# Kernel optimization log

Hardware: AMD Instinct MI355X
Metric: run time of the kernel (lower is better)

Reference implementation:

```python
import jax, jax.numpy as jnp
import numpy as np

B, L, D, H = 16, 4096, 512, 512
TEMP, THRESH, PRIOR = 1.0, 0.5, 0.25


def setup_inputs() -> dict:
    key = jax.random.key(0)
    k1, k2, k3, k4, k5 = jax.random.split(key, 5)
    hidden = jax.random.normal(k1, (B, L, D), jnp.float32)
    # variable-length sequences: lengths in [L/2, L]
    lengths = jax.random.randint(k2, (B,), L // 2, L + 1)
    attention_mask = (jnp.arange(L)[None, :] < lengths[:, None]).astype(jnp.float32)
    # uniform noise for RelaxedBernoulli rsample (logistic reparameterization)
    u = jax.random.uniform(k3, (B, L), jnp.float32, 1e-6, 1.0 - 1e-6)
    w1 = jax.random.normal(k4, (D, H), jnp.float32) * (1.0 / np.sqrt(D))
    b1 = jnp.zeros((H,), jnp.float32)
    w2 = jax.random.normal(k5, (H, 1), jnp.float32) * (1.0 / np.sqrt(H))
    b2 = jnp.full((1,), 3.0, jnp.float32)  # init_for_12: bias filled with +3
    return dict(hidden=hidden, attention_mask=attention_mask, u=u,
                w1=w1, b1=b1, w2=w2, b2=b2)


def _binomial_loss(k, n, p):
    # -log Binomial(n, p).pmf(k) / n
    log_coef = (jax.lax.lgamma(n + 1.0) - jax.lax.lgamma(k + 1.0)
                - jax.lax.lgamma(n - k + 1.0))
    return -(log_coef + k * jnp.log(p) + (n - k) * jnp.log1p(-p)) / n


def _forward(hidden, attention_mask, u, w1, b1, w2, b2):
    # boundary MLP -> logits (B, L)
    logits = (jax.nn.relu(hidden @ w1 + b1) @ w2 + b2)[..., 0]
    # RelaxedBernoulli(temp, probs=sigmoid(logits)).rsample():
    # sigmoid((logits + logistic_noise) / temp)
    logistic = jnp.log(u) - jnp.log1p(-u)
    soft = jax.nn.sigmoid((logits + logistic) / TEMP) * attention_mask
    hard = (soft > THRESH).astype(hidden.dtype) * attention_mask
    # force a boundary on the last real token of each sequence
    pad = attention_mask == 0
    first_pad = pad & (jnp.cumsum(pad.astype(jnp.int32), axis=1) == 1)
    last_real = jnp.roll(first_pad, -1, axis=1).at[:, -1].set(False).astype(hidden.dtype)
    hard = jnp.maximum(hard, last_real)
    soft = jnp.maximum(soft, last_real)
    # straight-through estimator
    hard_b = hard - jax.lax.stop_gradient(soft) + soft
    masked_hidden = hidden * attention_mask[..., None]
    # segment id of token t = #boundaries strictly before t (boundary closes its segment)
    hard_sg = jax.lax.stop_gradient(hard)
    seg = (jnp.cumsum(hard_sg, axis=1) - hard_sg).astype(jnp.int32)  # (B, L)

    def pool_one(x, sid):
        # x: (L, D), sid: (L,) -> mean pool per segment, padded to L segments
        s = jax.ops.segment_sum(x, sid, num_segments=L)
        c = jax.ops.segment_sum(jnp.ones((L,), x.dtype), sid, num_segments=L)
        return s / jnp.maximum(c, 1.0)[:, None]

    pooled = jax.vmap(pool_one)(masked_hidden, seg)  # (B, L, D), first nb[b] rows valid
    nb = hard_sg.sum(axis=1)  # per-example boundary count
    valid = jnp.arange(L)[None, :] < nb[:, None]
    pooled = pooled * valid[..., None]
    shortened_attention_mask = valid.astype(attention_mask.dtype)  # padded to L
    k = hard_b.sum()
    n = attention_mask.sum()
    loss = _binomial_loss(k, n, PRIOR)
    return pooled, loss, k, n, shortened_attention_mask


def reference(hidden, attention_mask, u, w1, b1, w2, b2):
    return _forward(hidden, attention_mask, u, w1, b1, w2, b2)
```

## Files before the change

kernel.cpp:

```cpp
#include <hip/hip_runtime.h>
#include <hip/hip_bf16.h>
#include <stdint.h>

#define BB 16
#define LL 4096
#define DD 512
#define HH 512
#define MM (BB * LL)
#define NTILES_H 8

typedef _Float16 f16x8 __attribute__((ext_vector_type(8)));
typedef float f32x4 __attribute__((ext_vector_type(4)));


__global__ __launch_bounds__(256) void conv_a_kernel(
    const float* __restrict__ A, _Float16* __restrict__ Ah, _Float16* __restrict__ Al)
{
    const int t    = blockIdx.x * 256 + threadIdx.x;
    const int tile = t >> 9;
    const int u    = t & 511;
    const int ml   = u >> 2;
    const int q    = u & 3;
    const int mt   = tile >> 4;
    const int kt   = tile & 15;
    const int g    = q ^ (ml & 3);

    const float* src = A + ((size_t)(mt * 128 + ml)) * DD + kt * 32;
    const float4 x = *reinterpret_cast<const float4*>(src + 4 * g);
    const float4 y = *reinterpret_cast<const float4*>(src + 16 + 4 * g);
    const float v[8] = {x.x, x.y, x.z, x.w, y.x, y.y, y.z, y.w};

    f16x8 h, l;
#pragma unroll
    for (int e = 0; e < 8; ++e) {
        const _Float16 hh = (_Float16)v[e];
        const float r = v[e] - (float)hh;
        h[e] = hh;
        l[e] = (_Float16)(r * 4096.0f);
    }
    *reinterpret_cast<f16x8*>(Ah + (size_t)tile * 4096 + u * 8) = h;
    *reinterpret_cast<f16x8*>(Al + (size_t)tile * 4096 + u * 8) = l;
}

__global__ __launch_bounds__(256) void conv_b_kernel(
    const float* __restrict__ W1, _Float16* __restrict__ Bh, _Float16* __restrict__ Bl)
{
    const int t    = blockIdx.x * 256 + threadIdx.x;
    const int tile = t >> 9;
    const int u    = t & 511;
    const int nl   = u >> 2;
    const int q    = u & 3;
    const int ht   = tile >> 4;
    const int kt   = tile & 15;
    const int g    = q ^ (nl & 3);

    const int n = ht * 128 + nl;
    const int kbase = kt * 32;
    f16x8 h, l;
#pragma unroll
    for (int e = 0; e < 8; ++e) {
        const int k = kbase + ((e < 4) ? (4 * g + e) : (16 + 4 * g + (e - 4)));
        const float v = W1[(size_t)k * HH + n] * 64.0f;
        const _Float16 hh = (_Float16)v;
        const float r = v - (float)hh;
        h[e] = hh;
        l[e] = (_Float16)(r * 4096.0f);
    }
    *reinterpret_cast<f16x8*>(Bh + (size_t)tile * 4096 + u * 8) = h;
    *reinterpret_cast<f16x8*>(Bl + (size_t)tile * 4096 + u * 8) = l;
}

__device__ __forceinline__ void gload16(const void* g, void* l)
{
    __builtin_amdgcn_global_load_lds(
        (const __attribute__((address_space(1))) unsigned int*)g,
        (__attribute__((address_space(3))) unsigned int*)l, 16, 0, 0);
}

__global__ __launch_bounds__(256, 2) void gemm_mfma_kernel(
    const _Float16* __restrict__ Ah, const _Float16* __restrict__ Al,
    const _Float16* __restrict__ Bh, const _Float16* __restrict__ Bl,
    const float* __restrict__ B1,    const float* __restrict__ W2,
    float* __restrict__ part)
{
    __shared__ __align__(16) char lds[2][4][8192];

    const int d  = blockIdx.x;
    const int x  = d & 7;
    const int ht = (d >> 3) & 3;
    const int mt = x * 64 + (d >> 5);

    const int tid  = threadIdx.x;
    const int lane = tid & 63;
    const int w    = tid >> 6;
    const int wr   = w >> 1;
    const int wc   = w & 1;
    const int c    = lane & 15;
    const int g    = lane >> 4;

    int aoff[4], boff[4];
#pragma unroll
    for (int f = 0; f < 4; ++f) {
        const int m_local = wr * 64 + f * 16 + c;
        aoff[f] = m_local * 64 + ((g ^ (c & 3)) << 4);
        const int n_local = wc * 64 + f * 16 + c;
        boff[f] = n_local * 64 + ((g ^ (c & 3)) << 4);
    }

    f32x4 accM[4][4] = {};
    f32x4 accL[4][4] = {};

    auto stage = [&](int kt, int b) {
        const _Float16* s0 = Ah + ((size_t)(mt * 16 + kt)) * 4096;
        const _Float16* s1 = Al + ((size_t)(mt * 16 + kt)) * 4096;
        const _Float16* s2 = Bh + ((size_t)(ht * 16 + kt)) * 4096;
        const _Float16* s3 = Bl + ((size_t)(ht * 16 + kt)) * 4096;
        char* l = &lds[b][0][0];
#pragma unroll
        for (int i = 0; i < 2; ++i) {
            const int e = (tid + i * 256) * 8;
            const int o = (tid + i * 256) * 16;
            gload16(s0 + e, l + 0 * 8192 + o);
            gload16(s1 + e, l + 1 * 8192 + o);
            gload16(s2 + e, l + 2 * 8192 + o);
            gload16(s3 + e, l + 3 * 8192 + o);
        }
    };

    stage(0, 0);
    int buf = 0;
    for (int kt = 0; kt < 16; ++kt) {
        __syncthreads();
        if (kt + 1 < 16) stage(kt + 1, buf ^ 1);
        const char* base = &lds[buf][0][0];
        f16x8 ah[4], al[4];
#pragma unroll
        for (int mf = 0; mf < 4; ++mf) {
            ah[mf] = *reinterpret_cast<const f16x8*>(base + 0 * 8192 + aoff[mf]);
            al[mf] = *reinterpret_cast<const f16x8*>(base + 1 * 8192 + aoff[mf]);
        }
#pragma unroll
        for (int nf = 0; nf < 4; ++nf) {
            const f16x8 bh = *reinterpret_cast<const f16x8*>(base + 2 * 8192 + boff[nf]);
            const f16x8 bl = *reinterpret_cast<const f16x8*>(base + 3 * 8192 + boff[nf]);
#pragma unroll
            for (int mf = 0; mf < 4; ++mf) {
                accM[mf][nf] = __builtin_amdgcn_mfma_f32_16x16x32_f16(ah[mf], bh, accM[mf][nf], 0, 0, 0);
                accL[mf][nf] = __builtin_amdgcn_mfma_f32_16x16x32_f16(ah[mf], bl, accL[mf][nf], 0, 0, 0);
                accL[mf][nf] = __builtin_amdgcn_mfma_f32_16x16x32_f16(al[mf], bh, accL[mf][nf], 0, 0, 0);
            }
        }
        buf ^= 1;
    }

    float w2v[4], b1v[4];
#pragma unroll
    for (int nf = 0; nf < 4; ++nf) {
        const int n = ht * 128 + wc * 64 + nf * 16 + c;
        w2v[nf] = W2[n];
        b1v[nf] = B1[n];
    }
    float red[4][4];
#pragma unroll
    for (int mf = 0; mf < 4; ++mf)
#pragma unroll
        for (int r = 0; r < 4; ++r) {
            float s = 0.0f;
#pragma unroll
            for (int nf = 0; nf < 4; ++nf) {
                float y = (accM[mf][nf][r] + accL[mf][nf][r] * (1.0f / 4096.0f)) * (1.0f / 64.0f) + b1v[nf];
                y = (y > 0.0f) ? y : 0.0f;
                s = fmaf(y, w2v[nf], s);
            }
            red[mf][r] = s;
        }
#pragma unroll
    for (int step = 1; step < 16; step <<= 1)
#pragma unroll
        for (int mf = 0; mf < 4; ++mf)
#pragma unroll
            for (int r = 0; r < 4; ++r)
                red[mf][r] += __shfl_xor(red[mf][r], step);
    if (c == 0) {
        const int p = ht * 2 + wc;
#pragma unroll
        for (int mf = 0; mf < 4; ++mf)
#pragma unroll
            for (int r = 0; r < 4; ++r) {
                const int m = mt * 128 + wr * 64 + mf * 16 + g * 4 + r;
                part[(size_t)p * MM + m] = red[mf][r];
            }
    }
}

#define BM 64
#define BN 64
#define BK 32

__global__ __launch_bounds__(256) void mlp_gemm_kernel(
    const float* __restrict__ A, const float* __restrict__ W1,
    const float* __restrict__ B1, const float* __restrict__ W2,
    float* __restrict__ part)
{
    __shared__ __align__(16) float As[BK][BM];
    __shared__ __align__(16) float Bs[BK][BN];
    __shared__ float red[64][17];

    const int ht = blockIdx.x;
    const int mt = blockIdx.y;
    const int t  = threadIdx.x;
    const int tx = t & 15;
    const int ty = t >> 4;
    const int row0 = mt * BM;
    const int n0   = ht * BN;

    float acc[4][4];
#pragma unroll
    for (int i = 0; i < 4; ++i)
#pragma unroll
        for (int j = 0; j < 4; ++j) acc[i][j] = 0.0f;

    for (int k0 = 0; k0 < DD; k0 += BK) {
#pragma unroll
        for (int i = 0; i < 2; ++i) {
            const int idx = t + i * 256;
            const int m   = idx >> 3;
            const int kq  = idx & 7;
            const float4 a = *reinterpret_cast<const float4*>(
                &A[(size_t)(row0 + m) * DD + k0 + kq * 4]);
            As[kq * 4 + 0][m] = a.x;
            As[kq * 4 + 1][m] = a.y;
            As[kq * 4 + 2][m] = a.z;
            As[kq * 4 + 3][m] = a.w;
        }
#pragma unroll
        for (int i = 0; i < 2; ++i) {
            const int idx = t + i * 256;
            const int kk  = idx >> 4;
            const int nq  = idx & 15;
            const float4 bv = *reinterpret_cast<const float4*>(
                &W1[(size_t)(k0 + kk) * HH + n0 + nq * 4]);
            *reinterpret_cast<float4*>(&Bs[kk][nq * 4]) = bv;
        }
        __syncthreads();
#pragma unroll
        for (int k = 0; k < BK; ++k) {
            const float4 av = *reinterpret_cast<const float4*>(&As[k][ty * 4]);
            const float4 bv = *reinterpret_cast<const float4*>(&Bs[k][tx * 4]);
            const float a[4]  = {av.x, av.y, av.z, av.w};
            const float bb[4] = {bv.x, bv.y, bv.z, bv.w};
#pragma unroll
            for (int i = 0; i < 4; ++i)
#pragma unroll
                for (int j = 0; j < 4; ++j)
                    acc[i][j] = fmaf(a[i], bb[j], acc[i][j]);
        }
        __syncthreads();
    }

    const float4 b1v = *reinterpret_cast<const float4*>(&B1[n0 + tx * 4]);
    const float4 w2v = *reinterpret_cast<const float4*>(&W2[n0 + tx * 4]);
    const float b1a[4] = {b1v.x, b1v.y, b1v.z, b1v.w};
    const float w2a[4] = {w2v.x, w2v.y, w2v.z, w2v.w};
#pragma unroll
    for (int i = 0; i < 4; ++i) {
        float p = 0.0f;
#pragma unroll
        for (int j = 0; j < 4; ++j) {
            float y = acc[i][j] + b1a[j];
            y = (y > 0.0f) ? y : 0.0f;
            p = fmaf(y, w2a[j], p);
        }
        red[ty * 4 + i][tx] = p;
    }
    __syncthreads();
    if (t < 64) {
        float s = 0.0f;
#pragma unroll
        for (int q = 0; q < 16; ++q) s += red[t][q];
        part[(size_t)(t & 0) * 0 + (size_t)blockIdx.x * MM + row0 + t] = s;
    }
}

__global__ __launch_bounds__(1024) void boundary_scan_kernel(
    const float* __restrict__ part, const float* __restrict__ mask,
    const float* __restrict__ u,    const float* __restrict__ b2,
    int* __restrict__ bpos, int* __restrict__ nb, int* __restrict__ lenb,
    float* __restrict__ smask_out)
{
    __shared__ int sdata[1024];
    __shared__ int s_len;
    const int b   = blockIdx.x;
    const int tid = threadIdx.x;
    const int base = b * LL;
    const float b2v = b2[0];

    float mv[4];
    int lm = 0;
#pragma unroll
    for (int j = 0; j < 4; ++j) {
        const int l = tid * 4 + j;
        mv[j] = mask[base + l];
        lm += (mv[j] != 0.0f) ? 1 : 0;
    }
    sdata[tid] = lm;
    __syncthreads();
    for (int off = 512; off > 0; off >>= 1) {
        if (tid < off) sdata[tid] += sdata[tid + off];
        __syncthreads();
    }
    if (tid == 0) s_len = sdata[0];
    __syncthreads();
    const int len = s_len;
    __syncthreads();

    int h[4];
    int cnt = 0;
#pragma unroll
    for (int j = 0; j < 4; ++j) {
        const int l = tid * 4 + j;
        float logit = b2v;
#pragma unroll
        for (int p = 0; p < NTILES_H; ++p) logit += part[(size_t)p * MM + base + l];
        const float uu = u[base + l];
        const float xx = logit + logf(uu) - log1pf(-uu);
        int hh = (xx > 0.0f && mv[j] != 0.0f) ? 1 : 0;
        if (len < LL && l == len - 1) hh = 1;
        h[j] = hh;
        cnt += hh;
    }

    sdata[tid] = cnt;
    __syncthreads();
    for (int off = 1; off < 1024; off <<= 1) {
        int v = (tid >= off) ? sdata[tid - off] : 0;
        __syncthreads();
        sdata[tid] += v;
        __syncthreads();
    }
    const int excl  = sdata[tid] - cnt;
    const int total = sdata[1023];

    int pos = excl;
#pragma unroll
    for (int j = 0; j < 4; ++j) {
        if (h[j]) {
            bpos[base + pos] = tid * 4 + j;
            ++pos;
        }
    }
    if (tid == 0) {
        nb[b]   = total;
        lenb[b] = len;
    }
#pragma unroll
    for (int j = 0; j < 4; ++j) {
        const int l = tid * 4 + j;
        smask_out[base + l] = (l < total) ? 1.0f : 0.0f;
    }
}

__global__ __launch_bounds__(128) void pool_kernel(
    const float* __restrict__ hidden, const int* __restrict__ bpos,
    const int* __restrict__ nb, float* __restrict__ out)
{
    const int blk = blockIdx.x;
    const int b   = blk >> 12;
    const int s   = blk & (LL - 1);
    const int tid = threadIdx.x;
    const int base = b * LL;

    float ax = 0.0f, ay = 0.0f, az = 0.0f, aw = 0.0f;
    const int n = nb[b];
    if (s < n) {
        const int start = (s == 0) ? 0 : (bpos[base + s - 1] + 1);
        const int end   = bpos[base + s];
        const float inv = 1.0f / (float)(end - start + 1);
        for (int tkn = start; tkn <= end; ++tkn) {
            const float4 v = *reinterpret_cast<const float4*>(
                &hidden[((size_t)(base + tkn)) * DD + tid * 4]);
            ax += v.x; ay += v.y; az += v.z; aw += v.w;
        }
        ax *= inv; ay *= inv; az *= inv; aw *= inv;
    }
    float4 r; r.x = ax; r.y = ay; r.z = az; r.w = aw;
    *reinterpret_cast<float4*>(&out[((size_t)(base + s)) * DD + tid * 4]) = r;
}

__global__ void finalize_kernel(
    const int* __restrict__ nb, const int* __restrict__ lenb,
    float* __restrict__ out)
{
    if (threadIdx.x == 0 && blockIdx.x == 0) {
        int k = 0, n = 0;
        for (int b = 0; b < BB; ++b) { k += nb[b]; n += lenb[b]; }
        const double dk = (double)k, dn = (double)n, p = 0.25;
        const double logc = lgamma(dn + 1.0) - lgamma(dk + 1.0) - lgamma(dn - dk + 1.0);
        const double loss = -(logc + dk * log(p) + (dn - dk) * log1p(-p)) / dn;
        out[0] = (float)loss;
        out[1] = (float)k;
        out[2] = (float)n;
    }
}

extern "C" void kernel_launch(void* const* d_in, const int* in_sizes, int n_in,
                              void* d_out, int out_size, void* d_ws, size_t ws_size,
                              hipStream_t stream) {
    const float* hidden = (const float*)d_in[0];
    const float* mask   = (const float*)d_in[1];
    const float* u      = (const float*)d_in[2];
    const float* w1     = (const float*)d_in[3];
    const float* b1     = (const float*)d_in[4];
    const float* w2     = (const float*)d_in[5];
    const float* b2     = (const float*)d_in[6];
    float* out = (float*)d_out;

    const size_t AH_BYTES = (size_t)8192 * 4096 * 2;
    const size_t BH_BYTES = (size_t)64 * 4096 * 2;
    const size_t PART_BYTES = (size_t)NTILES_H * MM * 4;
    const size_t BPOS_BYTES = (size_t)MM * 4;
    const size_t need = AH_BYTES * 2 + BH_BYTES * 2 + PART_BYTES + BPOS_BYTES + 128;

    const size_t P = (size_t)MM * DD;
    float* smask = out + P + 3;

    char* ws = (char*)d_ws;
    float* part; int* bpos; int* nbuf; int* lenb;

    if (ws_size >= need) {
        _Float16* Ah = (_Float16*)ws;
        _Float16* Al = (_Float16*)(ws + AH_BYTES);
        _Float16* Bh = (_Float16*)(ws + AH_BYTES * 2);
        _Float16* Bl = (_Float16*)(ws + AH_BYTES * 2 + BH_BYTES);
        part = (float*)(ws + AH_BYTES * 2 + BH_BYTES * 2);
        bpos = (int*)(ws + AH_BYTES * 2 + BH_BYTES * 2 + PART_BYTES);
        nbuf = (int*)(ws + AH_BYTES * 2 + BH_BYTES * 2 + PART_BYTES + BPOS_BYTES);
        lenb = nbuf + BB;

        conv_a_kernel<<<16384, 256, 0, stream>>>(hidden, Ah, Al);
        conv_b_kernel<<<128, 256, 0, stream>>>(w1, Bh, Bl);
        gemm_mfma_kernel<<<2048, 256, 0, stream>>>(Ah, Al, Bh, Bl, b1, w2, part);
    } else {
        part = (float*)ws;
        bpos = (int*)(ws + PART_BYTES);
        nbuf = (int*)(ws + PART_BYTES + BPOS_BYTES);
        lenb = nbuf + BB;
        mlp_gemm_kernel<<<dim3(NTILES_H, MM / BM), 256, 0, stream>>>(hidden, w1, b1, w2, part);
    }

    boundary_scan_kernel<<<BB, 1024, 0, stream>>>(part, mask, u, b2, bpos, nbuf, lenb, smask);
    pool_kernel<<<MM, 128, 0, stream>>>(hidden, bpos, nbuf, out);
    finalize_kernel<<<1, 64, 0, stream>>>(nbuf, lenb, out + P);
}
```

Before: 398.2 us.

## Parallelize boundary scan across chunks and strengthen LDS swizzle for MFMA tiles

The single-block-per-sequence boundary scan is replaced by three kernels. A binary-search length kernel finds each sequence length. A 256-block flags kernel computes hard boundaries with per-chunk ballot counts. A 256-block scan kernel compacts boundary positions using chunk prefix sums and wave ballots. This aims to remove the long, serial-ish 1024-thread Hillis-Steele scan that ran on only 16 blocks. Separately, the fp16 tile swizzle gains an extra XOR term in both the conversion kernels and the GEMM LDS addressing, to reduce LDS bank conflicts. The binary search relies on the mask being a contiguous prefix of ones.

```diff
diff --git a/kernel.cpp b/kernel.cpp
--- a/kernel.cpp
+++ b/kernel.cpp
@@ -23,7 +23,7 @@
     const int q    = u & 3;
     const int mt   = tile >> 4;
     const int kt   = tile & 15;
-    const int g    = q ^ (ml & 3);
+    const int g    = q ^ (ml & 3) ^ ((ml >> 2) & 3);
 
     const float* src = A + ((size_t)(mt * 128 + ml)) * DD + kt * 32;
     const float4 x = *reinterpret_cast<const float4*>(src + 4 * g);
@@ -52,7 +52,7 @@
     const int q    = u & 3;
     const int ht   = tile >> 4;
     const int kt   = tile & 15;
-    const int g    = q ^ (nl & 3);
+    const int g    = q ^ (nl & 3) ^ ((nl >> 2) & 3);
 
     const int n = ht * 128 + nl;
     const int kbase = kt * 32;
@@ -98,13 +98,14 @@
     const int c    = lane & 15;
     const int g    = lane >> 4;
 
+    const int q = g ^ (c & 3) ^ ((c >> 2) & 3);
     int aoff[4], boff[4];
 #pragma unroll
     for (int f = 0; f < 4; ++f) {
         const int m_local = wr * 64 + f * 16 + c;
-        aoff[f] = m_local * 64 + ((g ^ (c & 3)) << 4);
+        aoff[f] = m_local * 64 + (q << 4);
         const int n_local = wc * 64 + f * 16 + c;
-        boff[f] = n_local * 64 + ((g ^ (c & 3)) << 4);
+        boff[f] = n_local * 64 + (q << 4);
     }
 
     f32x4 accM[4][4] = {};
@@ -278,86 +279,94 @@
         float s = 0.0f;
 #pragma unroll
         for (int q = 0; q < 16; ++q) s += red[t][q];
-        part[(size_t)(t & 0) * 0 + (size_t)blockIdx.x * MM + row0 + t] = s;
-    }
-}
-
-__global__ __launch_bounds__(1024) void boundary_scan_kernel(
-    const float* __restrict__ part, const float* __restrict__ mask,
-    const float* __restrict__ u,    const float* __restrict__ b2,
-    int* __restrict__ bpos, int* __restrict__ nb, int* __restrict__ lenb,
-    float* __restrict__ smask_out)
-{
-    __shared__ int sdata[1024];
-    __shared__ int s_len;
-    const int b   = blockIdx.x;
-    const int tid = threadIdx.x;
-    const int base = b * LL;
-    const float b2v = b2[0];
-
-    float mv[4];
-    int lm = 0;
-#pragma unroll
-    for (int j = 0; j < 4; ++j) {
-        const int l = tid * 4 + j;
-        mv[j] = mask[base + l];
-        lm += (mv[j] != 0.0f) ? 1 : 0;
-    }
-    sdata[tid] = lm;
+        part[(size_t)ht * MM + row0 + t] = s;
+    }
+}
+
+
+__global__ void len_kernel(const float* __restrict__ mask, int* __restrict__ lenb)
+{
+    const int b = threadIdx.x;
+    if (b < BB) {
+        const float* row = mask + b * LL;
+        int lo = 0, hi = LL;
+        while (lo < hi) {
+            const int mid = (lo + hi) >> 1;
+            if (row[mid] == 0.0f) hi = mid; else lo = mid + 1;
+        }
+        lenb[b] = lo;
+    }
+}
+
+__global__ __launch_bounds__(256) void flags_kernel(
+    const float* __restrict__ part, const float* __restrict__ u,
+    const float* __restrict__ b2,   const int* __restrict__ lenb,
+    int* __restrict__ flags, int* __restrict__ chunkcnt)
+{
+    __shared__ int wsum[4];
+    const int m   = blockIdx.x * 256 + threadIdx.x;
+    const int b   = m >> 12;
+    const int l   = m & (LL - 1);
+    const int len = lenb[b];
+
+    float logit = b2[0];
+#pragma unroll
+    for (int p = 0; p < NTILES_H; ++p) logit += part[(size_t)p * MM + m];
+    const float uu = u[m];
+    const float xx = logit + logf(uu) - log1pf(-uu);
+
+    int hh = (xx > 0.0f && l < len) ? 1 : 0;
+    if (len < LL && l == len - 1) hh = 1;
+    flags[m] = hh;
+
+    const unsigned long long bal = __ballot(hh);
+    const int lane = threadIdx.x & 63;
+    const int wid  = threadIdx.x >> 6;
+    if (lane == 0) wsum[wid] = __popcll(bal);
     __syncthreads();
-    for (int off = 512; off > 0; off >>= 1) {
-        if (tid < off) sdata[tid] += sdata[tid + off];
-        __syncthreads();
-    }
-    if (tid == 0) s_len = sdata[0];
+    if (threadIdx.x == 0)
+        chunkcnt[blockIdx.x] = wsum[0] + wsum[1] + wsum[2] + wsum[3];
+}
+
+__global__ __launch_bounds__(256) void scan_kernel(
+    const int* __restrict__ flags, const int* __restrict__ chunkcnt,
+    int* __restrict__ bpos, int* __restrict__ nb, float* __restrict__ smask_out)
+{
+    __shared__ int s_chunk[16];
+    __shared__ int wsum[4];
+    const int bid   = blockIdx.x;
+    const int b     = bid >> 4;
+    const int chunk = bid & 15;
+    const int tid   = threadIdx.x;
+    const int m     = bid * 256 + tid;
+    const int l     = m & (LL - 1);
+
+    if (tid < 16) s_chunk[tid] = chunkcnt[b * 16 + tid];
+
+    const int hh = flags[m];
+    const unsigned long long bal = __ballot(hh);
+    const int lane = tid & 63;
+    const int wid  = tid >> 6;
+    if (lane == 0) wsum[wid] = __popcll(bal);
     __syncthreads();
-    const int len = s_len;
-    __syncthreads();
-
-    int h[4];
-    int cnt = 0;
-#pragma unroll
-    for (int j = 0; j < 4; ++j) {
-        const int l = tid * 4 + j;
-        float logit = b2v;
-#pragma unroll
-        for (int p = 0; p < NTILES_H; ++p) logit += part[(size_t)p * MM + base + l];
-        const float uu = u[base + l];
-        const float xx = logit + logf(uu) - log1pf(-uu);
-        int hh = (xx > 0.0f && mv[j] != 0.0f) ? 1 : 0;
-        if (len < LL && l == len - 1) hh = 1;
-        h[j] = hh;
-        cnt += hh;
-    }
-
-    sdata[tid] = cnt;
-    __syncthreads();
-    for (int off = 1; off < 1024; off <<= 1) {
-        int v = (tid >= off) ? sdata[tid - off] : 0;
-        __syncthreads();
-        sdata[tid] += v;
-        __syncthreads();
-    }
-    const int excl  = sdata[tid] - cnt;
-    const int total = sdata[1023];
-
-    int pos = excl;
-#pragma unroll
-    for (int j = 0; j < 4; ++j) {
-        if (h[j]) {
-            bpos[base + pos] = tid * 4 + j;
-            ++pos;
-        }
-    }
-    if (tid == 0) {
-        nb[b]   = total;
-        lenb[b] = len;
-    }
-#pragma unroll
-    for (int j = 0; j < 4; ++j) {
-        const int l = tid * 4 + j;
-        smask_out[base + l] = (l < total) ? 1.0f : 0.0f;
-    }
+
+    int pre = 0, tot = 0;
+#pragma unroll
+    for (int i = 0; i < 16; ++i) {
+        const int ci = s_chunk[i];
+        pre += (i < chunk) ? ci : 0;
+        tot += ci;
+    }
+    int woff = 0;
+#pragma unroll
+    for (int i = 0; i < 4; ++i) woff += (i < wid) ? wsum[i] : 0;
+
+    if (hh) {
+        const int excl = __popcll(bal & ((1ull << lane) - 1ull));
+        bpos[b * LL + pre + woff + excl] = l;
+    }
+    smask_out[m] = (l < tot) ? 1.0f : 0.0f;
+    if (chunk == 0 && tid == 0) nb[b] = tot;
 }
 
 __global__ __launch_bounds__(128) void pool_kernel(
@@ -415,40 +424,46 @@
     const float* b2     = (const float*)d_in[6];
     float* out = (float*)d_out;
 
-    const size_t AH_BYTES = (size_t)8192 * 4096 * 2;
-    const size_t BH_BYTES = (size_t)64 * 4096 * 2;
+    const size_t AH_BYTES   = (size_t)8192 * 4096 * 2;
+    const size_t BH_BYTES   = (size_t)64 * 4096 * 2;
     const size_t PART_BYTES = (size_t)NTILES_H * MM * 4;
     const size_t BPOS_BYTES = (size_t)MM * 4;
-    const size_t need = AH_BYTES * 2 + BH_BYTES * 2 + PART_BYTES + BPOS_BYTES + 128;
+    const size_t FLAG_BYTES = (size_t)MM * 4;
+    const size_t need = AH_BYTES * 2 + BH_BYTES * 2 + PART_BYTES + BPOS_BYTES + FLAG_BYTES + 4096;
 
     const size_t P = (size_t)MM * DD;
     float* smask = out + P + 3;
 
     char* ws = (char*)d_ws;
-    float* part; int* bpos; int* nbuf; int* lenb;
-
-    if (ws_size >= need) {
+    float* part; int* bpos; int* flags; int* chunkcnt; int* nbuf; int* lenb;
+    bool fast = (ws_size >= need);
+
+    char* tail;
+    if (fast) tail = ws + AH_BYTES * 2 + BH_BYTES * 2;
+    else      tail = ws;
+    part     = (float*)tail;
+    bpos     = (int*)(tail + PART_BYTES);
+    flags    = (int*)(tail + PART_BYTES + BPOS_BYTES);
+    chunkcnt = (int*)(tail + PART_BYTES + BPOS_BYTES + FLAG_BYTES);
+    nbuf     = chunkcnt + 256;
+    lenb     = nbuf + BB;
+
+    len_kernel<<<1, 64, 0, stream>>>(mask, lenb);
+
+    if (fast) {
         _Float16* Ah = (_Float16*)ws;
         _Float16* Al = (_Float16*)(ws + AH_BYTES);
         _Float16* Bh = (_Float16*)(ws + AH_BYTES * 2);
         _Float16* Bl = (_Float16*)(ws + AH_BYTES * 2 + BH_BYTES);
-        part = (float*)(ws + AH_BYTES * 2 + BH_BYTES * 2);
-        bpos = (int*)(ws + AH_BYTES * 2 + BH_BYTES * 2 + PART_BYTES);
-        nbuf = (int*)(ws + AH_BYTES * 2 + BH_BYTES * 2 + PART_BYTES + BPOS_BYTES);
-        lenb = nbuf + BB;
-
+        conv_b_kernel<<<128, 256, 0, stream>>>(w1, Bh, Bl);
         conv_a_kernel<<<16384, 256, 0, stream>>>(hidden, Ah, Al);
-        conv_b_kernel<<<128, 256, 0, stream>>>(w1, Bh, Bl);
         gemm_mfma_kernel<<<2048, 256, 0, stream>>>(Ah, Al, Bh, Bl, b1, w2, part);
     } else {
-        part = (float*)ws;
-        bpos = (int*)(ws + PART_BYTES);
-        nbuf = (int*)(ws + PART_BYTES + BPOS_BYTES);
-        lenb = nbuf + BB;
         mlp_gemm_kernel<<<dim3(NTILES_H, MM / BM), 256, 0, stream>>>(hidden, w1, b1, w2, part);
     }
 
-    boundary_scan_kernel<<<BB, 1024, 0, stream>>>(part, mask, u, b2, bpos, nbuf, lenb, smask);
+    flags_kernel<<<256, 256, 0, stream>>>(part, u, b2, lenb, flags, chunkcnt);
+    scan_kernel<<<256, 256, 0, stream>>>(flags, chunkcnt, bpos, nbuf, smask);
     pool_kernel<<<MM, 128, 0, stream>>>(hidden, bpos, nbuf, out);
     finalize_kernel<<<1, 64, 0, stream>>>(nbuf, lenb, out + P);
 }
```

Result: no change. 397.8 us (-0.1%).

## Fuse fp32-to-fp16 split of hidden into GEMM tile load and simplify scan

Applied to the files above, without the earlier changes.

Drops the separate conversion pass that split the hidden activations into high/low fp16 copies in workspace. The GEMM now loads raw fp32 tiles into LDS and does the split in registers, which removes a full read and two half-size writes of the 128MB activation tensor. Mask lengths are now found by a binary search inside the weight-conversion launch, and the row scan uses wavefront shuffle scans instead of an LDS Hillis-Steele loop. The cost is larger fp32 LDS tiles, more conversion ALU work inside the MFMA loop, and a changed swizzle pattern. The binary search assumes the mask is a contiguous prefix of ones.

```diff
diff --git a/kernel.cpp b/kernel.cpp
--- a/kernel.cpp
+++ b/kernel.cpp
@@ -12,39 +12,23 @@
 typedef _Float16 f16x8 __attribute__((ext_vector_type(8)));
 typedef float f32x4 __attribute__((ext_vector_type(4)));
 
-
-__global__ __launch_bounds__(256) void conv_a_kernel(
-    const float* __restrict__ A, _Float16* __restrict__ Ah, _Float16* __restrict__ Al)
-{
-    const int t    = blockIdx.x * 256 + threadIdx.x;
-    const int tile = t >> 9;
-    const int u    = t & 511;
-    const int ml   = u >> 2;
-    const int q    = u & 3;
-    const int mt   = tile >> 4;
-    const int kt   = tile & 15;
-    const int g    = q ^ (ml & 3);
-
-    const float* src = A + ((size_t)(mt * 128 + ml)) * DD + kt * 32;
-    const float4 x = *reinterpret_cast<const float4*>(src + 4 * g);
-    const float4 y = *reinterpret_cast<const float4*>(src + 16 + 4 * g);
-    const float v[8] = {x.x, x.y, x.z, x.w, y.x, y.y, y.z, y.w};
-
-    f16x8 h, l;
-#pragma unroll
-    for (int e = 0; e < 8; ++e) {
-        const _Float16 hh = (_Float16)v[e];
-        const float r = v[e] - (float)hh;
-        h[e] = hh;
-        l[e] = (_Float16)(r * 4096.0f);
-    }
-    *reinterpret_cast<f16x8*>(Ah + (size_t)tile * 4096 + u * 8) = h;
-    *reinterpret_cast<f16x8*>(Al + (size_t)tile * 4096 + u * 8) = l;
-}
-
-__global__ __launch_bounds__(256) void conv_b_kernel(
-    const float* __restrict__ W1, _Float16* __restrict__ Bh, _Float16* __restrict__ Bl)
-{
+__global__ __launch_bounds__(256) void convb_len_kernel(
+    const float* __restrict__ W1, _Float16* __restrict__ Bh, _Float16* __restrict__ Bl,
+    const float* __restrict__ mask, int* __restrict__ lenb)
+{
+    if (blockIdx.x == 128) {
+        const int b = threadIdx.x;
+        if (b < BB) {
+            const float* row = mask + b * LL;
+            int lo = 0, hi = LL;
+            while (lo < hi) {
+                const int mid = (lo + hi) >> 1;
+                if (row[mid] == 0.0f) hi = mid; else lo = mid + 1;
+            }
+            lenb[b] = lo;
+        }
+        return;
+    }
     const int t    = blockIdx.x * 256 + threadIdx.x;
     const int tile = t >> 9;
     const int u    = t & 511;
@@ -52,7 +36,7 @@
     const int q    = u & 3;
     const int ht   = tile >> 4;
     const int kt   = tile & 15;
-    const int g    = q ^ (nl & 3);
+    const int g    = q ^ (nl & 3) ^ ((nl >> 2) & 3);
 
     const int n = ht * 128 + nl;
     const int kbase = kt * 32;
@@ -78,12 +62,12 @@
 }
 
 __global__ __launch_bounds__(256, 2) void gemm_mfma_kernel(
-    const _Float16* __restrict__ Ah, const _Float16* __restrict__ Al,
+    const float* __restrict__ A,
     const _Float16* __restrict__ Bh, const _Float16* __restrict__ Bl,
     const float* __restrict__ B1,    const float* __restrict__ W2,
     float* __restrict__ part)
 {
-    __shared__ __align__(16) char lds[2][4][8192];
+    __shared__ __align__(16) char lds[2][32768];
 
     const int d  = blockIdx.x;
     const int x  = d & 7;
@@ -98,32 +82,37 @@
     const int c    = lane & 15;
     const int g    = lane >> 4;
 
-    int aoff[4], boff[4];
+    int aoff0[4], aoff1[4], boff[4];
+    const int qb = g ^ (c & 3) ^ ((c >> 2) & 3);
 #pragma unroll
     for (int f = 0; f < 4; ++f) {
-        const int m_local = wr * 64 + f * 16 + c;
-        aoff[f] = m_local * 64 + ((g ^ (c & 3)) << 4);
+        const int r = wr * 64 + f * 16 + c;
+        aoff0[f] = r * 128 + ((g ^ (c & 7)) << 4);
+        aoff1[f] = r * 128 + (((g + 4) ^ (c & 7)) << 4);
         const int n_local = wc * 64 + f * 16 + c;
-        boff[f] = n_local * 64 + ((g ^ (c & 3)) << 4);
+        boff[f] = n_local * 64 + (qb << 4);
     }
 
     f32x4 accM[4][4] = {};
     f32x4 accL[4][4] = {};
 
-    auto stage = [&](int kt, int b) {
-        const _Float16* s0 = Ah + ((size_t)(mt * 16 + kt)) * 4096;
-        const _Float16* s1 = Al + ((size_t)(mt * 16 + kt)) * 4096;
+    auto stage = [&](int kt, int bsel) {
+        char* l = &lds[bsel][0];
+#pragma unroll
+        for (int i = 0; i < 4; ++i) {
+            const int s   = tid + i * 256;
+            const int row = s >> 3;
+            const int kc  = (s & 7) ^ (row & 7);
+            gload16(A + ((size_t)(mt * 128 + row)) * DD + kt * 32 + kc * 4,
+                    l + s * 16);
+        }
         const _Float16* s2 = Bh + ((size_t)(ht * 16 + kt)) * 4096;
         const _Float16* s3 = Bl + ((size_t)(ht * 16 + kt)) * 4096;
-        char* l = &lds[b][0][0];
 #pragma unroll
         for (int i = 0; i < 2; ++i) {
-            const int e = (tid + i * 256) * 8;
-            const int o = (tid + i * 256) * 16;
-            gload16(s0 + e, l + 0 * 8192 + o);
-            gload16(s1 + e, l + 1 * 8192 + o);
-            gload16(s2 + e, l + 2 * 8192 + o);
-            gload16(s3 + e, l + 3 * 8192 + o);
+            const int s = tid + i * 256;
+            gload16(s2 + s * 8, l + 16384 + s * 16);
+            gload16(s3 + s * 8, l + 24576 + s * 16);
         }
     };
 
@@ -132,17 +121,28 @@
     for (int kt = 0; kt < 16; ++kt) {
         __syncthreads();
         if (kt + 1 < 16) stage(kt + 1, buf ^ 1);
-        const char* base = &lds[buf][0][0];
+        const char* base = &lds[buf][0];
+
         f16x8 ah[4], al[4];
 #pragma unroll
         for (int mf = 0; mf < 4; ++mf) {
-            ah[mf] = *reinterpret_cast<const f16x8*>(base + 0 * 8192 + aoff[mf]);
-            al[mf] = *reinterpret_cast<const f16x8*>(base + 1 * 8192 + aoff[mf]);
+            const f32x4 v0 = *reinterpret_cast<const f32x4*>(base + aoff0[mf]);
+            const f32x4 v1 = *reinterpret_cast<const f32x4*>(base + aoff1[mf]);
+            const float v[8] = {v0[0], v0[1], v0[2], v0[3], v1[0], v1[1], v1[2], v1[3]};
+            f16x8 h, lo;
+#pragma unroll
+            for (int e = 0; e < 8; ++e) {
+                const _Float16 hh = (_Float16)v[e];
+                h[e]  = hh;
+                lo[e] = (_Float16)((v[e] - (float)hh) * 4096.0f);
+            }
+            ah[mf] = h;
+            al[mf] = lo;
         }
 #pragma unroll
         for (int nf = 0; nf < 4; ++nf) {
-            const f16x8 bh = *reinterpret_cast<const f16x8*>(base + 2 * 8192 + boff[nf]);
-            const f16x8 bl = *reinterpret_cast<const f16x8*>(base + 3 * 8192 + boff[nf]);
+            const f16x8 bh = *reinterpret_cast<const f16x8*>(base + 16384 + boff[nf]);
+            const f16x8 bl = *reinterpret_cast<const f16x8*>(base + 24576 + boff[nf]);
 #pragma unroll
             for (int mf = 0; mf < 4; ++mf) {
                 accM[mf][nf] = __builtin_amdgcn_mfma_f32_16x16x32_f16(ah[mf], bh, accM[mf][nf], 0, 0, 0);
@@ -278,41 +278,23 @@
         float s = 0.0f;
 #pragma unroll
         for (int q = 0; q < 16; ++q) s += red[t][q];
-        part[(size_t)(t & 0) * 0 + (size_t)blockIdx.x * MM + row0 + t] = s;
-    }
-}
-
-__global__ __launch_bounds__(1024) void boundary_scan_kernel(
-    const float* __restrict__ part, const float* __restrict__ mask,
-    const float* __restrict__ u,    const float* __restrict__ b2,
-    int* __restrict__ bpos, int* __restrict__ nb, int* __restrict__ lenb,
-    float* __restrict__ smask_out)
-{
-    __shared__ int sdata[1024];
-    __shared__ int s_len;
-    const int b   = blockIdx.x;
-    const int tid = threadIdx.x;
+        part[(size_t)ht * MM + row0 + t] = s;
+    }
+}
+
+__global__ __launch_bounds__(1024) void rowscan_kernel(
+    const float* __restrict__ part, const float* __restrict__ u,
+    const float* __restrict__ b2,   const int* __restrict__ lenb,
+    int* __restrict__ bpos, int* __restrict__ nb, float* __restrict__ smask_out)
+{
+    __shared__ int wtot[16];
+    const int b    = blockIdx.x;
+    const int tid  = threadIdx.x;
+    const int lane = tid & 63;
+    const int wid  = tid >> 6;
     const int base = b * LL;
+    const int len  = lenb[b];
     const float b2v = b2[0];
-
-    float mv[4];
-    int lm = 0;
-#pragma unroll
-    for (int j = 0; j < 4; ++j) {
-        const int l = tid * 4 + j;
-        mv[j] = mask[base + l];
-        lm += (mv[j] != 0.0f) ? 1 : 0;
-    }
-    sdata[tid] = lm;
-    __syncthreads();
-    for (int off = 512; off > 0; off >>= 1) {
-        if (tid < off) sdata[tid] += sdata[tid + off];
-        __syncthreads();
-    }
-    if (tid == 0) s_len = sdata[0];
-    __syncthreads();
-    const int len = s_len;
-    __syncthreads();
 
     int h[4];
     int cnt = 0;
@@ -324,24 +306,30 @@
         for (int p = 0; p < NTILES_H; ++p) logit += part[(size_t)p * MM + base + l];
         const float uu = u[base + l];
         const float xx = logit + logf(uu) - log1pf(-uu);
-        int hh = (xx > 0.0f && mv[j] != 0.0f) ? 1 : 0;
+        int hh = (xx > 0.0f && l < len) ? 1 : 0;
         if (len < LL && l == len - 1) hh = 1;
         h[j] = hh;
         cnt += hh;
     }
 
-    sdata[tid] = cnt;
+    int incl = cnt;
+#pragma unroll
+    for (int s = 1; s < 64; s <<= 1) {
+        const int v = __shfl_up(incl, s);
+        if (lane >= s) incl += v;
+    }
+    if (lane == 63) wtot[wid] = incl;
     __syncthreads();
-    for (int off = 1; off < 1024; off <<= 1) {
-        int v = (tid >= off) ? sdata[tid - off] : 0;
-        __syncthreads();
-        sdata[tid] += v;
-        __syncthreads();
-    }
-    const int excl  = sdata[tid] - cnt;
-    const int total = sdata[1023];
-
-    int pos = excl;
+
+    int woff = 0, tot = 0;
+#pragma unroll
+    for (int i = 0; i < 16; ++i) {
+        const int wi = wtot[i];
+        woff += (i < wid) ? wi : 0;
+        tot  += wi;
+    }
+
+    int pos = woff + incl - cnt;
 #pragma unroll
     for (int j = 0; j < 4; ++j) {
         if (h[j]) {
@@ -349,15 +337,12 @@
             ++pos;
         }
     }
-    if (tid == 0) {
-        nb[b]   = total;
-        lenb[b] = len;
-    }
 #pragma unroll
     for (int j = 0; j < 4; ++j) {
         const int l = tid * 4 + j;
-        smask_out[base + l] = (l < total) ? 1.0f : 0.0f;
-    }
+        smask_out[base + l] = (l < tot) ? 1.0f : 0.0f;
+    }
+    if (tid == 0) nb[b] = tot;
 }
 
 __global__ __launch_bounds__(128) void pool_kernel(
@@ -415,40 +400,34 @@
     const float* b2     = (const float*)d_in[6];
     float* out = (float*)d_out;
 
-    const size_t AH_BYTES = (size_t)8192 * 4096 * 2;
-    const size_t BH_BYTES = (size_t)64 * 4096 * 2;
+    const size_t BH_BYTES   = (size_t)64 * 4096 * 2;
     const size_t PART_BYTES = (size_t)NTILES_H * MM * 4;
     const size_t BPOS_BYTES = (size_t)MM * 4;
-    const size_t need = AH_BYTES * 2 + BH_BYTES * 2 + PART_BYTES + BPOS_BYTES + 128;
+    const size_t need = BH_BYTES * 2 + PART_BYTES + BPOS_BYTES + 4096;
 
     const size_t P = (size_t)MM * DD;
     float* smask = out + P + 3;
 
     char* ws = (char*)d_ws;
-    float* part; int* bpos; int* nbuf; int* lenb;
-
-    if (ws_size >= need) {
-        _Float16* Ah = (_Float16*)ws;
-        _Float16* Al = (_Float16*)(ws + AH_BYTES);
-        _Float16* Bh = (_Float16*)(ws + AH_BYTES * 2);
-        _Float16* Bl = (_Float16*)(ws + AH_BYTES * 2 + BH_BYTES);
-        part = (float*)(ws + AH_BYTES * 2 + BH_BYTES * 2);
-        bpos = (int*)(ws + AH_BYTES * 2 + BH_BYTES * 2 + PART_BYTES);
-        nbuf = (int*)(ws + AH_BYTES * 2 + BH_BYTES * 2 + PART_BYTES + BPOS_BYTES);
-        lenb = nbuf + BB;
-
-        conv_a_kernel<<<16384, 256, 0, stream>>>(hidden, Ah, Al);
-        conv_b_kernel<<<128, 256, 0, stream>>>(w1, Bh, Bl);
-        gemm_mfma_kernel<<<2048, 256, 0, stream>>>(Ah, Al, Bh, Bl, b1, w2, part);
+    const bool fast = (ws_size >= need);
+
+    char* tail = fast ? (ws + BH_BYTES * 2) : ws;
+    float* part = (float*)tail;
+    int*   bpos = (int*)(tail + PART_BYTES);
+    int*   nbuf = (int*)(tail + PART_BYTES + BPOS_BYTES);
+    int*   lenb = nbuf + BB;
+
+    if (fast) {
+        _Float16* Bh = (_Float16*)ws;
+        _Float16* Bl = (_Float16*)(ws + BH_BYTES);
+        convb_len_kernel<<<129, 256, 0, stream>>>(w1, Bh, Bl, mask, lenb);
+        gemm_mfma_kernel<<<2048, 256, 0, stream>>>(hidden, Bh, Bl, b1, w2, part);
     } else {
-        part = (float*)ws;
-        bpos = (int*)(ws + PART_BYTES);
-        nbuf = (int*)(ws + PART_BYTES + BPOS_BYTES);
-        lenb = nbuf + BB;
+        convb_len_kernel<<<129, 256, 0, stream>>>(w1, (_Float16*)ws, (_Float16*)ws, mask, lenb);
         mlp_gemm_kernel<<<dim3(NTILES_H, MM / BM), 256, 0, stream>>>(hidden, w1, b1, w2, part);
     }
 
-    boundary_scan_kernel<<<BB, 1024, 0, stream>>>(part, mask, u, b2, bpos, nbuf, lenb, smask);
+    rowscan_kernel<<<BB, 1024, 0, stream>>>(part, u, b2, lenb, bpos, nbuf, smask);
     pool_kernel<<<MM, 128, 0, stream>>>(hidden, bpos, nbuf, out);
     finalize_kernel<<<1, 64, 0, stream>>>(nbuf, lenb, out + P);
 }
```

Measured after the change: 332.3 us. 1.2x faster.
